# Kernel tuning notes

Hardware: AMD Instinct MI355X
Metric: run time of the kernel (lower is better)

## Reference

```python
import jax, jax.numpy as jnp
import numpy as np

N = 50000
E = 800000
D_IN, D_HID, D_OUT = 128, 128, 256


def _sage_layer(x, src, dst, W_l, b_l, W_r):
    # PyG SAGEConv: out = lin_l(mean_j x_j) + lin_r(x_i)
    msg = x[src]                                              # [E, d]
    agg = jax.ops.segment_sum(msg, dst, num_segments=x.shape[0])
    cnt = jax.ops.segment_sum(jnp.ones((src.shape[0],), x.dtype), dst,
                              num_segments=x.shape[0])
    mean = agg / jnp.maximum(cnt, 1.0)[:, None]
    return mean @ W_l.T + b_l + x @ W_r.T


def setup_inputs() -> dict:
    key = jax.random.key(0)
    ks = jax.random.split(key, 12)
    x = jax.random.normal(ks[0], (N, D_IN), dtype=jnp.float32)
    edge_index = jax.random.randint(ks[1], (2, E), 0, N, dtype=jnp.int64)

    def lin(k, out_d, in_d):
        s = 1.0 / np.sqrt(in_d)
        return jax.random.uniform(k, (out_d, in_d), jnp.float32, -s, s)

    return {
        "x": x,
        "edge_index": edge_index,
        "W_l0": lin(ks[2], D_HID, D_IN),
        "b_l0": jnp.zeros((D_HID,), jnp.float32),
        "W_r0": lin(ks[3], D_HID, D_IN),
        "W_l1": lin(ks[4], D_HID, D_HID),
        "b_l1": jnp.zeros((D_HID,), jnp.float32),
        "W_r1": lin(ks[5], D_HID, D_HID),
        "W_l2": lin(ks[6], D_OUT, D_HID),
        "b_l2": jnp.zeros((D_OUT,), jnp.float32),
        "W_r2": lin(ks[7], D_OUT, D_HID),
    }


def reference(x, edge_index, W_l0, b_l0, W_r0, W_l1, b_l1, W_r1, W_l2, b_l2, W_r2):
    src, dst = edge_index[0], edge_index[1]
    h = jax.nn.relu(_sage_layer(x, src, dst, W_l0, b_l0, W_r0))   # dropout = identity (eval)
    h = jax.nn.relu(_sage_layer(h, src, dst, W_l1, b_l1, W_r1))
    out = _sage_layer(h, src, dst, W_l2, b_l2, W_r2)
    return out
```

## Files before the change

kernel.cpp:

```cpp
#include <hip/hip_runtime.h>
#include <stdint.h>

typedef unsigned short u16;
typedef unsigned int   u32;
typedef __attribute__((ext_vector_type(8))) short short8;
typedef __attribute__((ext_vector_type(4))) float f32x4;

__device__ __forceinline__ u16 f2bf(float f) {
    u32 u = __float_as_uint(f);
    u32 r = (u + 0x7FFFu + ((u >> 16) & 1u)) >> 16;
    return (u16)r;
}

__global__ void detect_fmt(const int* __restrict__ ei, int* __restrict__ flag) {
    if (blockIdx.x == 0 && threadIdx.x == 0) {
        int z = ei[1] | ei[3] | ei[5] | ei[7] | ei[9] | ei[11];
        flag[0] = (z == 0) ? 1 : 0;
    }
}

__global__ void zero_out(float* __restrict__ p, size_t n) {
    size_t i = (size_t)blockIdx.x * 256 + threadIdx.x;
    size_t stride = (size_t)gridDim.x * 256;
    for (; i < n; i += stride) p[i] = 0.f;
}

__global__ void count_deg(const int* __restrict__ ei, const int* __restrict__ flag,
                          int* __restrict__ deg, int E, int N) {
    int e = blockIdx.x * 256 + threadIdx.x;
    if (e >= E) return;
    int dst = flag[0] ? ei[2 * E + 2 * e] : ei[E + e];
    dst = min(max(dst, 0), N - 1);
    atomicAdd(&deg[dst], 1);
}

__global__ void scan_partial(const int* __restrict__ deg, int* __restrict__ bsum, int N) {
    __shared__ int sh[256];
    int t = threadIdx.x;
    int idx0 = blockIdx.x * 1024 + t * 4;
    int s = 0;
    #pragma unroll
    for (int i = 0; i < 4; ++i) { int idx = idx0 + i; if (idx < N) s += deg[idx]; }
    sh[t] = s;
    __syncthreads();
    #pragma unroll
    for (int off = 128; off > 0; off >>= 1) {
        if (t < off) sh[t] += sh[t + off];
        __syncthreads();
    }
    if (t == 0) bsum[blockIdx.x] = sh[0];
}

__global__ void scan_bsum(int* __restrict__ bsum, int nb,
                          int* __restrict__ offs, int N) {
    __shared__ int sh[256];
    __shared__ int carry;
    int t = threadIdx.x;
    if (t == 0) carry = 0;
    __syncthreads();
    for (int base = 0; base < nb; base += 256) {
        int v = (base + t < nb) ? bsum[base + t] : 0;
        sh[t] = v;
        __syncthreads();
        #pragma unroll
        for (int off = 1; off < 256; off <<= 1) {
            int x = (t >= off) ? sh[t - off] : 0;
            __syncthreads();
            sh[t] += x;
            __syncthreads();
        }
        if (base + t < nb) bsum[base + t] = carry + sh[t] - v;
        __syncthreads();
        if (t == 255) carry += sh[255];
        __syncthreads();
    }
    if (t == 0) offs[N] = carry;
}

__global__ void scan_final(int* __restrict__ deg, const int* __restrict__ bsum,
                           int* __restrict__ offs, int N) {
    __shared__ int sh[256];
    int t = threadIdx.x;
    int idx0 = blockIdx.x * 1024 + t * 4;
    int v[4];
    int s = 0;
    #pragma unroll
    for (int i = 0; i < 4; ++i) {
        int idx = idx0 + i;
        v[i] = (idx < N) ? deg[idx] : 0;
        s += v[i];
    }
    sh[t] = s;
    __syncthreads();
    #pragma unroll
    for (int off = 1; off < 256; off <<= 1) {
        int x = (t >= off) ? sh[t - off] : 0;
        __syncthreads();
        sh[t] += x;
        __syncthreads();
    }
    int run = sh[t] - s + bsum[blockIdx.x];
    #pragma unroll
    for (int i = 0; i < 4; ++i) {
        int idx = idx0 + i;
        if (idx < N) { offs[idx] = run; deg[idx] = run; }
        run += v[i];
    }
}

__global__ void bucket_edges(const int* __restrict__ ei, const int* __restrict__ flag,
                             int* __restrict__ cursor, int* __restrict__ ssrc,
                             int E, int N) {
    int e = blockIdx.x * 256 + threadIdx.x;
    if (e >= E) return;
    int is64 = flag[0];
    int src = is64 ? ei[2 * e] : ei[e];
    int dst = is64 ? ei[2 * E + 2 * e] : ei[E + e];
    src = min(max(src, 0), N - 1);
    dst = min(max(dst, 0), N - 1);
    int p = atomicAdd(&cursor[dst], 1);
    if (p >= 0 && p < E) ssrc[p] = src;
}

__global__ void conv_bf16(const float4* __restrict__ x, uint2* __restrict__ H, int n4) {
    int i = blockIdx.x * 256 + threadIdx.x;
    if (i >= n4) return;
    float4 v = x[i];
    uint2 o;
    o.x = ((u32)f2bf(v.y) << 16) | f2bf(v.x);
    o.y = ((u32)f2bf(v.w) << 16) | f2bf(v.z);
    H[i] = o;
}

__global__ void prep_w(const float* __restrict__ Wl, const float* __restrict__ Wr,
                       u16* __restrict__ Wc, int dout) {
    int i = blockIdx.x * 256 + threadIdx.x;
    if (i >= dout * 256) return;
    int j = i >> 8, k = i & 255;
    float v = (k < 128) ? Wl[j * 128 + k] : Wr[j * 128 + (k - 128)];
    Wc[i] = f2bf(v);
}

__global__ void aggregate(const u16* __restrict__ H, const int* __restrict__ offs,
                          const int* __restrict__ ssrc, u16* __restrict__ M, int N) {
    int node = blockIdx.x * 16 + (threadIdx.x >> 4);
    int sub  = threadIdx.x & 15;
    if (node >= N) return;
    int beg = offs[node], end = offs[node + 1];
    float a0[8] = {}, a1[8] = {};
    int j = beg;
    for (; j + 1 < end; j += 2) {
        int s0 = ssrc[j], s1 = ssrc[j + 1];
        uint4 p0 = *(const uint4*)(H + (size_t)s0 * 128 + sub * 8);
        uint4 p1 = *(const uint4*)(H + (size_t)s1 * 128 + sub * 8);
        a0[0] += __uint_as_float(p0.x << 16); a0[1] += __uint_as_float(p0.x & 0xFFFF0000u);
        a0[2] += __uint_as_float(p0.y << 16); a0[3] += __uint_as_float(p0.y & 0xFFFF0000u);
        a0[4] += __uint_as_float(p0.z << 16); a0[5] += __uint_as_float(p0.z & 0xFFFF0000u);
        a0[6] += __uint_as_float(p0.w << 16); a0[7] += __uint_as_float(p0.w & 0xFFFF0000u);
        a1[0] += __uint_as_float(p1.x << 16); a1[1] += __uint_as_float(p1.x & 0xFFFF0000u);
        a1[2] += __uint_as_float(p1.y << 16); a1[3] += __uint_as_float(p1.y & 0xFFFF0000u);
        a1[4] += __uint_as_float(p1.z << 16); a1[5] += __uint_as_float(p1.z & 0xFFFF0000u);
        a1[6] += __uint_as_float(p1.w << 16); a1[7] += __uint_as_float(p1.w & 0xFFFF0000u);
    }
    if (j < end) {
        int s0 = ssrc[j];
        uint4 p0 = *(const uint4*)(H + (size_t)s0 * 128 + sub * 8);
        a0[0] += __uint_as_float(p0.x << 16); a0[1] += __uint_as_float(p0.x & 0xFFFF0000u);
        a0[2] += __uint_as_float(p0.y << 16); a0[3] += __uint_as_float(p0.y & 0xFFFF0000u);
        a0[4] += __uint_as_float(p0.z << 16); a0[5] += __uint_as_float(p0.z & 0xFFFF0000u);
        a0[6] += __uint_as_float(p0.w << 16); a0[7] += __uint_as_float(p0.w & 0xFFFF0000u);
    }
    int d = end - beg;
    float sc = 1.f / (float)(d > 0 ? d : 1);
    uint4 o;
    o.x = ((u32)f2bf((a0[1]+a1[1])*sc) << 16) | f2bf((a0[0]+a1[0])*sc);
    o.y = ((u32)f2bf((a0[3]+a1[3])*sc) << 16) | f2bf((a0[2]+a1[2])*sc);
    o.z = ((u32)f2bf((a0[5]+a1[5])*sc) << 16) | f2bf((a0[4]+a1[4])*sc);
    o.w = ((u32)f2bf((a0[7]+a1[7])*sc) << 16) | f2bf((a0[6]+a1[6])*sc);
    *(uint4*)(M + (size_t)node * 128 + sub * 8) = o;
}

template<int DOUT, bool RELU, bool OUT_F32>
__global__ void gemm_mfma(const u16* __restrict__ M, const u16* __restrict__ H,
                          const u16* __restrict__ Wc, const float* __restrict__ bias,
                          void* __restrict__ out, int N) {
    int tid  = threadIdx.x;
    int w    = tid >> 6;
    int l    = tid & 63;
    int m_base = blockIdx.x * 128 + w * 32;
    int n_base = blockIdx.y * 128;

    int lr = l & 15;
    int lq = l >> 4;
    int kof = lq * 8;

    f32x4 acc[2][8];
    #pragma unroll
    for (int i = 0; i < 2; ++i)
        #pragma unroll
        for (int j = 0; j < 8; ++j) acc[i][j] = (f32x4){0.f, 0.f, 0.f, 0.f};

    int r0 = m_base + lr, r1 = r0 + 16;
    const short8 zf = (short8){0,0,0,0,0,0,0,0};

    #pragma unroll
    for (int ks = 0; ks < 8; ++ks) {
        const u16* Asrc = (ks < 4) ? M : H;
        int ka = (ks & 3) * 32 + kof;
        short8 a0 = (r0 < N) ? *(const short8*)(Asrc + (size_t)r0 * 128 + ka) : zf;
        short8 a1 = (r1 < N) ? *(const short8*)(Asrc + (size_t)r1 * 128 + ka) : zf;
        int kb = ks * 32 + kof;
        #pragma unroll
        for (int ct = 0; ct < 8; ++ct) {
            int wrow = n_base + ct * 16 + lr;
            short8 b = *(const short8*)(Wc + (size_t)wrow * 256 + kb);
            acc[0][ct] = __builtin_amdgcn_mfma_f32_16x16x32_bf16(a0, b, acc[0][ct], 0, 0, 0);
            acc[1][ct] = __builtin_amdgcn_mfma_f32_16x16x32_bf16(a1, b, acc[1][ct], 0, 0, 0);
        }
    }

    #pragma unroll
    for (int rg = 0; rg < 2; ++rg) {
        #pragma unroll
        for (int ct = 0; ct < 8; ++ct) {
            int col = n_base + ct * 16 + lr;
            float bv = bias[col];
            #pragma unroll
            for (int i = 0; i < 4; ++i) {
                int row = m_base + rg * 16 + lq * 4 + i;
                if (row >= N) continue;
                float v = acc[rg][ct][i] + bv;
                if (RELU) v = fmaxf(v, 0.f);
                if (OUT_F32) ((float*)out)[(size_t)row * DOUT + col] = v;
                else         ((u16*)out)[(size_t)row * DOUT + col] = f2bf(v);
            }
        }
    }
}

extern "C" void kernel_launch(void* const* d_in, const int* in_sizes, int n_in,
                              void* d_out, int out_size, void* d_ws, size_t ws_size,
                              hipStream_t stream) {
    const float* x   = (const float*)d_in[0];
    const int*   ei  = (const int*)d_in[1];
    const float* Wl0 = (const float*)d_in[2];
    const float* bl0 = (const float*)d_in[3];
    const float* Wr0 = (const float*)d_in[4];
    const float* Wl1 = (const float*)d_in[5];
    const float* bl1 = (const float*)d_in[6];
    const float* Wr1 = (const float*)d_in[7];
    const float* Wl2 = (const float*)d_in[8];
    const float* bl2 = (const float*)d_in[9];
    const float* Wr2 = (const float*)d_in[10];

    const int N = in_sizes[0] / 128;
    const int E = in_sizes[1] / 2;

    size_t off = 0;
    auto alloc = [&](size_t bytes) -> size_t {
        size_t p = off;
        off += (bytes + 255) & ~(size_t)255;
        return p;
    };
    size_t o_flag = alloc(256);
    size_t o_deg  = alloc((size_t)N * 4);
    size_t o_offs = alloc(((size_t)N + 1) * 4);
    size_t o_ssrc = alloc((size_t)E * 4);
    size_t o_bsum = alloc((((size_t)N + 1023) / 1024) * 4);
    size_t o_Hx   = alloc((size_t)N * 128 * 2);
    size_t o_Ha   = alloc((size_t)N * 128 * 2);
    size_t o_Hb   = alloc((size_t)N * 128 * 2);
    size_t o_Mb   = alloc((size_t)N * 128 * 2);
    size_t o_Wc0  = alloc((size_t)128 * 256 * 2);
    size_t o_Wc1  = alloc((size_t)128 * 256 * 2);
    size_t o_Wc2  = alloc((size_t)256 * 256 * 2);

    if (off > ws_size) {
        zero_out<<<2048, 256, 0, stream>>>((float*)d_out, (size_t)out_size);
        return;
    }

    char* ws = (char*)d_ws;
    int* flag = (int*)(ws + o_flag);
    int* deg  = (int*)(ws + o_deg);
    int* offs = (int*)(ws + o_offs);
    int* ssrc = (int*)(ws + o_ssrc);
    int* bsum = (int*)(ws + o_bsum);
    u16* Hx   = (u16*)(ws + o_Hx);
    u16* Ha   = (u16*)(ws + o_Ha);
    u16* Hb   = (u16*)(ws + o_Hb);
    u16* Mb   = (u16*)(ws + o_Mb);
    u16* Wc0  = (u16*)(ws + o_Wc0);
    u16* Wc1  = (u16*)(ws + o_Wc1);
    u16* Wc2  = (u16*)(ws + o_Wc2);

    hipMemsetAsync(deg, 0, (size_t)N * 4, stream);
    detect_fmt<<<1, 64, 0, stream>>>(ei, flag);

    int eb = (E + 255) / 256;
    int nb = (N + 1023) / 1024;
    count_deg<<<eb, 256, 0, stream>>>(ei, flag, deg, E, N);
    scan_partial<<<nb, 256, 0, stream>>>(deg, bsum, N);
    scan_bsum<<<1, 256, 0, stream>>>(bsum, nb, offs, N);
    scan_final<<<nb, 256, 0, stream>>>(deg, bsum, offs, N);
    bucket_edges<<<eb, 256, 0, stream>>>(ei, flag, deg, ssrc, E, N);

    int n4 = N * 32;
    conv_bf16<<<(n4 + 255) / 256, 256, 0, stream>>>((const float4*)x, (uint2*)Hx, n4);
    prep_w<<<(128 * 256 + 255) / 256, 256, 0, stream>>>(Wl0, Wr0, Wc0, 128);
    prep_w<<<(128 * 256 + 255) / 256, 256, 0, stream>>>(Wl1, Wr1, Wc1, 128);
    prep_w<<<(256 * 256 + 255) / 256, 256, 0, stream>>>(Wl2, Wr2, Wc2, 256);

    int ab = (N + 15) / 16;
    dim3 g1((N + 127) / 128, 1), g2((N + 127) / 128, 2);

    aggregate<<<ab, 256, 0, stream>>>(Hx, offs, ssrc, Mb, N);
    gemm_mfma<128, true, false><<<g1, 256, 0, stream>>>(Mb, Hx, Wc0, bl0, Ha, N);
    aggregate<<<ab, 256, 0, stream>>>(Ha, offs, ssrc, Mb, N);
    gemm_mfma<128, true, false><<<g1, 256, 0, stream>>>(Mb, Ha, Wc1, bl1, Hb, N);
    aggregate<<<ab, 256, 0, stream>>>(Hb, offs, ssrc, Mb, N);
    gemm_mfma<256, false, true><<<g2, 256, 0, stream>>>(Mb, Hb, Wc2, bl2, d_out, N);
}
```

Before: 390.6 us.

## Replace global-atomic CSR build with two-pass shared-memory radix bucketing

Builds the destination-sorted CSR with a two-level bucket sort instead of global atomics. Each chunk first takes a shared-memory histogram over 256-node buckets, then scatters (src,dst) pairs into bucket ranges, and a per-bucket kernel sorts them by node using shared-memory atomics. This removes heavy global atomic contention on the per-node degree and cursor arrays, at the cost of an extra E*8-byte pairs buffer and one more pass over the edges. It also unrolls the aggregation gather loop to four independent loads per iteration to raise memory-level parallelism.

```diff
diff --git a/kernel.cpp b/kernel.cpp
--- a/kernel.cpp
+++ b/kernel.cpp
@@ -6,16 +6,20 @@
 typedef __attribute__((ext_vector_type(8))) short short8;
 typedef __attribute__((ext_vector_type(4))) float f32x4;
 
+#define CHUNK 8192
+
 __device__ __forceinline__ u16 f2bf(float f) {
     u32 u = __float_as_uint(f);
     u32 r = (u + 0x7FFFu + ((u >> 16) & 1u)) >> 16;
     return (u16)r;
 }
 
-__global__ void detect_fmt(const int* __restrict__ ei, int* __restrict__ flag) {
+__global__ void detect_fmt(const int* __restrict__ ei, int* __restrict__ flag,
+                           int* __restrict__ offs, int N, int E) {
     if (blockIdx.x == 0 && threadIdx.x == 0) {
         int z = ei[1] | ei[3] | ei[5] | ei[7] | ei[9] | ei[11];
         flag[0] = (z == 0) ? 1 : 0;
+        offs[N] = E;
     }
 }
 
@@ -25,22 +29,31 @@
     for (; i < n; i += stride) p[i] = 0.f;
 }
 
-__global__ void count_deg(const int* __restrict__ ei, const int* __restrict__ flag,
-                          int* __restrict__ deg, int E, int N) {
-    int e = blockIdx.x * 256 + threadIdx.x;
-    if (e >= E) return;
-    int dst = flag[0] ? ei[2 * E + 2 * e] : ei[E + e];
-    dst = min(max(dst, 0), N - 1);
-    atomicAdd(&deg[dst], 1);
-}
-
-__global__ void scan_partial(const int* __restrict__ deg, int* __restrict__ bsum, int N) {
+__global__ void hist_bucket(const int* __restrict__ ei, const int* __restrict__ flag,
+                            int* __restrict__ cnt, int E, int N, int nb, int NBK) {
+    __shared__ int h[256];
+    int b = blockIdx.x, t = threadIdx.x;
+    h[t] = 0;
+    __syncthreads();
+    int is64 = flag[0];
+    int base = b * CHUNK;
+    int endE = min(base + CHUNK, E);
+    for (int i = base + t; i < endE; i += 256) {
+        int dst = is64 ? ei[2 * E + 2 * i] : ei[E + i];
+        dst = min(max(dst, 0), N - 1);
+        atomicAdd(&h[dst >> 8], 1);
+    }
+    __syncthreads();
+    for (int B = t; B < NBK; B += 256) cnt[B * nb + b] = h[B];
+}
+
+__global__ void scan_partial(const int* __restrict__ a, int* __restrict__ bsum, int M) {
     __shared__ int sh[256];
     int t = threadIdx.x;
     int idx0 = blockIdx.x * 1024 + t * 4;
     int s = 0;
     #pragma unroll
-    for (int i = 0; i < 4; ++i) { int idx = idx0 + i; if (idx < N) s += deg[idx]; }
+    for (int i = 0; i < 4; ++i) { int idx = idx0 + i; if (idx < M) s += a[idx]; }
     sh[t] = s;
     __syncthreads();
     #pragma unroll
@@ -51,15 +64,14 @@
     if (t == 0) bsum[blockIdx.x] = sh[0];
 }
 
-__global__ void scan_bsum(int* __restrict__ bsum, int nb,
-                          int* __restrict__ offs, int N) {
+__global__ void scan_bsum(int* __restrict__ bsum, int nbs) {
     __shared__ int sh[256];
     __shared__ int carry;
     int t = threadIdx.x;
     if (t == 0) carry = 0;
     __syncthreads();
-    for (int base = 0; base < nb; base += 256) {
-        int v = (base + t < nb) ? bsum[base + t] : 0;
+    for (int base = 0; base < nbs; base += 256) {
+        int v = (base + t < nbs) ? bsum[base + t] : 0;
         sh[t] = v;
         __syncthreads();
         #pragma unroll
@@ -69,16 +81,14 @@
             sh[t] += x;
             __syncthreads();
         }
-        if (base + t < nb) bsum[base + t] = carry + sh[t] - v;
+        if (base + t < nbs) bsum[base + t] = carry + sh[t] - v;
         __syncthreads();
         if (t == 255) carry += sh[255];
         __syncthreads();
     }
-    if (t == 0) offs[N] = carry;
-}
-
-__global__ void scan_final(int* __restrict__ deg, const int* __restrict__ bsum,
-                           int* __restrict__ offs, int N) {
+}
+
+__global__ void scan_final(int* __restrict__ a, const int* __restrict__ bsum, int M) {
     __shared__ int sh[256];
     int t = threadIdx.x;
     int idx0 = blockIdx.x * 1024 + t * 4;
@@ -87,7 +97,7 @@
     #pragma unroll
     for (int i = 0; i < 4; ++i) {
         int idx = idx0 + i;
-        v[i] = (idx < N) ? deg[idx] : 0;
+        v[i] = (idx < M) ? a[idx] : 0;
         s += v[i];
     }
     sh[t] = s;
@@ -103,23 +113,67 @@
     #pragma unroll
     for (int i = 0; i < 4; ++i) {
         int idx = idx0 + i;
-        if (idx < N) { offs[idx] = run; deg[idx] = run; }
+        if (idx < M) a[idx] = run;
         run += v[i];
     }
 }
 
-__global__ void bucket_edges(const int* __restrict__ ei, const int* __restrict__ flag,
-                             int* __restrict__ cursor, int* __restrict__ ssrc,
-                             int E, int N) {
-    int e = blockIdx.x * 256 + threadIdx.x;
-    if (e >= E) return;
+__global__ void scatter_pairs(const int* __restrict__ ei, const int* __restrict__ flag,
+                              const int* __restrict__ pboff, int2* __restrict__ pairs,
+                              int E, int N, int nb, int NBK) {
+    __shared__ int cur[256];
+    int b = blockIdx.x, t = threadIdx.x;
+    for (int B = t; B < NBK; B += 256) cur[B] = pboff[B * nb + b];
+    __syncthreads();
     int is64 = flag[0];
-    int src = is64 ? ei[2 * e] : ei[e];
-    int dst = is64 ? ei[2 * E + 2 * e] : ei[E + e];
-    src = min(max(src, 0), N - 1);
-    dst = min(max(dst, 0), N - 1);
-    int p = atomicAdd(&cursor[dst], 1);
-    if (p >= 0 && p < E) ssrc[p] = src;
+    int base = b * CHUNK;
+    int endE = min(base + CHUNK, E);
+    for (int i = base + t; i < endE; i += 256) {
+        int src = is64 ? ei[2 * i] : ei[i];
+        int dst = is64 ? ei[2 * E + 2 * i] : ei[E + i];
+        src = min(max(src, 0), N - 1);
+        dst = min(max(dst, 0), N - 1);
+        int slot = atomicAdd(&cur[dst >> 8], 1);
+        pairs[slot] = make_int2(src, dst);
+    }
+}
+
+__global__ void fine_sort(const int2* __restrict__ pairs, const int* __restrict__ pboff,
+                          int* __restrict__ offs, int* __restrict__ ssrc,
+                          int E, int N, int nb, int NBK) {
+    __shared__ int hist[256];
+    __shared__ int excl[256];
+    __shared__ int cur[256];
+    int B = blockIdx.x, t = threadIdx.x;
+    int rs = pboff[B * nb];
+    int re = (B + 1 < NBK) ? pboff[(B + 1) * nb] : E;
+    hist[t] = 0;
+    __syncthreads();
+    for (int i = rs + t; i < re; i += 256) {
+        int2 p = pairs[i];
+        atomicAdd(&hist[p.y & 255], 1);
+    }
+    __syncthreads();
+    int v = hist[t];
+    excl[t] = v;
+    __syncthreads();
+    #pragma unroll
+    for (int off = 1; off < 256; off <<= 1) {
+        int x = (t >= off) ? excl[t - off] : 0;
+        __syncthreads();
+        excl[t] += x;
+        __syncthreads();
+    }
+    int ex = excl[t] - v;
+    int node = B * 256 + t;
+    if (node < N) offs[node] = rs + ex;
+    cur[t] = rs + ex;
+    __syncthreads();
+    for (int i = rs + t; i < re; i += 256) {
+        int2 p = pairs[i];
+        int slot = atomicAdd(&cur[p.y & 255], 1);
+        ssrc[slot] = p.x;
+    }
 }
 
 __global__ void conv_bf16(const float4* __restrict__ x, uint2* __restrict__ H, int n4) {
@@ -141,42 +195,42 @@
     Wc[i] = f2bf(v);
 }
 
+__device__ __forceinline__ void acc8(float* a, uint4 p) {
+    a[0] += __uint_as_float(p.x << 16); a[1] += __uint_as_float(p.x & 0xFFFF0000u);
+    a[2] += __uint_as_float(p.y << 16); a[3] += __uint_as_float(p.y & 0xFFFF0000u);
+    a[4] += __uint_as_float(p.z << 16); a[5] += __uint_as_float(p.z & 0xFFFF0000u);
+    a[6] += __uint_as_float(p.w << 16); a[7] += __uint_as_float(p.w & 0xFFFF0000u);
+}
+
 __global__ void aggregate(const u16* __restrict__ H, const int* __restrict__ offs,
                           const int* __restrict__ ssrc, u16* __restrict__ M, int N) {
     int node = blockIdx.x * 16 + (threadIdx.x >> 4);
     int sub  = threadIdx.x & 15;
     if (node >= N) return;
     int beg = offs[node], end = offs[node + 1];
-    float a0[8] = {}, a1[8] = {};
+    float a0[8] = {}, a1[8] = {}, a2[8] = {}, a3[8] = {};
     int j = beg;
-    for (; j + 1 < end; j += 2) {
-        int s0 = ssrc[j], s1 = ssrc[j + 1];
+    for (; j + 3 < end; j += 4) {
+        int s0 = ssrc[j], s1 = ssrc[j + 1], s2 = ssrc[j + 2], s3 = ssrc[j + 3];
         uint4 p0 = *(const uint4*)(H + (size_t)s0 * 128 + sub * 8);
         uint4 p1 = *(const uint4*)(H + (size_t)s1 * 128 + sub * 8);
-        a0[0] += __uint_as_float(p0.x << 16); a0[1] += __uint_as_float(p0.x & 0xFFFF0000u);
-        a0[2] += __uint_as_float(p0.y << 16); a0[3] += __uint_as_float(p0.y & 0xFFFF0000u);
-        a0[4] += __uint_as_float(p0.z << 16); a0[5] += __uint_as_float(p0.z & 0xFFFF0000u);
-        a0[6] += __uint_as_float(p0.w << 16); a0[7] += __uint_as_float(p0.w & 0xFFFF0000u);
-        a1[0] += __uint_as_float(p1.x << 16); a1[1] += __uint_as_float(p1.x & 0xFFFF0000u);
-        a1[2] += __uint_as_float(p1.y << 16); a1[3] += __uint_as_float(p1.y & 0xFFFF0000u);
-        a1[4] += __uint_as_float(p1.z << 16); a1[5] += __uint_as_float(p1.z & 0xFFFF0000u);
-        a1[6] += __uint_as_float(p1.w << 16); a1[7] += __uint_as_float(p1.w & 0xFFFF0000u);
-    }
-    if (j < end) {
-        int s0 = ssrc[j];
-        uint4 p0 = *(const uint4*)(H + (size_t)s0 * 128 + sub * 8);
-        a0[0] += __uint_as_float(p0.x << 16); a0[1] += __uint_as_float(p0.x & 0xFFFF0000u);
-        a0[2] += __uint_as_float(p0.y << 16); a0[3] += __uint_as_float(p0.y & 0xFFFF0000u);
-        a0[4] += __uint_as_float(p0.z << 16); a0[5] += __uint_as_float(p0.z & 0xFFFF0000u);
-        a0[6] += __uint_as_float(p0.w << 16); a0[7] += __uint_as_float(p0.w & 0xFFFF0000u);
+        uint4 p2 = *(const uint4*)(H + (size_t)s2 * 128 + sub * 8);
+        uint4 p3 = *(const uint4*)(H + (size_t)s3 * 128 + sub * 8);
+        acc8(a0, p0); acc8(a1, p1); acc8(a2, p2); acc8(a3, p3);
+    }
+    for (; j < end; ++j) {
+        uint4 p0 = *(const uint4*)(H + (size_t)ssrc[j] * 128 + sub * 8);
+        acc8(a0, p0);
     }
     int d = end - beg;
     float sc = 1.f / (float)(d > 0 ? d : 1);
+    #pragma unroll
+    for (int i = 0; i < 8; ++i) a0[i] = (a0[i] + a1[i] + a2[i] + a3[i]) * sc;
     uint4 o;
-    o.x = ((u32)f2bf((a0[1]+a1[1])*sc) << 16) | f2bf((a0[0]+a1[0])*sc);
-    o.y = ((u32)f2bf((a0[3]+a1[3])*sc) << 16) | f2bf((a0[2]+a1[2])*sc);
-    o.z = ((u32)f2bf((a0[5]+a1[5])*sc) << 16) | f2bf((a0[4]+a1[4])*sc);
-    o.w = ((u32)f2bf((a0[7]+a1[7])*sc) << 16) | f2bf((a0[6]+a1[6])*sc);
+    o.x = ((u32)f2bf(a0[1]) << 16) | f2bf(a0[0]);
+    o.y = ((u32)f2bf(a0[3]) << 16) | f2bf(a0[2]);
+    o.z = ((u32)f2bf(a0[5]) << 16) | f2bf(a0[4]);
+    o.w = ((u32)f2bf(a0[7]) << 16) | f2bf(a0[6]);
     *(uint4*)(M + (size_t)node * 128 + sub * 8) = o;
 }
 
@@ -256,54 +310,59 @@
     const int N = in_sizes[0] / 128;
     const int E = in_sizes[1] / 2;
 
+    const int NBK = (N + 255) >> 8;
+    const int nb  = (E + CHUNK - 1) / CHUNK;
+    const int M_  = NBK * nb;
+    const int nbs = (M_ + 1023) / 1024;
+
     size_t off = 0;
     auto alloc = [&](size_t bytes) -> size_t {
         size_t p = off;
         off += (bytes + 255) & ~(size_t)255;
         return p;
     };
-    size_t o_flag = alloc(256);
-    size_t o_deg  = alloc((size_t)N * 4);
-    size_t o_offs = alloc(((size_t)N + 1) * 4);
-    size_t o_ssrc = alloc((size_t)E * 4);
-    size_t o_bsum = alloc((((size_t)N + 1023) / 1024) * 4);
-    size_t o_Hx   = alloc((size_t)N * 128 * 2);
-    size_t o_Ha   = alloc((size_t)N * 128 * 2);
-    size_t o_Hb   = alloc((size_t)N * 128 * 2);
-    size_t o_Mb   = alloc((size_t)N * 128 * 2);
-    size_t o_Wc0  = alloc((size_t)128 * 256 * 2);
-    size_t o_Wc1  = alloc((size_t)128 * 256 * 2);
-    size_t o_Wc2  = alloc((size_t)256 * 256 * 2);
-
-    if (off > ws_size) {
+    size_t o_flag  = alloc(256);
+    size_t o_cnt   = alloc((size_t)M_ * 4);
+    size_t o_bsum  = alloc((size_t)nbs * 4);
+    size_t o_offs  = alloc(((size_t)N + 1) * 4);
+    size_t o_ssrc  = alloc((size_t)E * 4);
+    size_t o_pairs = alloc((size_t)E * 8);
+    size_t o_Hx    = alloc((size_t)N * 128 * 2);
+    size_t o_Ha    = alloc((size_t)N * 128 * 2);
+    size_t o_Hb    = alloc((size_t)N * 128 * 2);
+    size_t o_Mb    = alloc((size_t)N * 128 * 2);
+    size_t o_Wc0   = alloc((size_t)128 * 256 * 2);
+    size_t o_Wc1   = alloc((size_t)128 * 256 * 2);
+    size_t o_Wc2   = alloc((size_t)256 * 256 * 2);
+
+    if (off > ws_size || NBK > 256) {
         zero_out<<<2048, 256, 0, stream>>>((float*)d_out, (size_t)out_size);
         return;
     }
 
     char* ws = (char*)d_ws;
-    int* flag = (int*)(ws + o_flag);
-    int* deg  = (int*)(ws + o_deg);
-    int* offs = (int*)(ws + o_offs);
-    int* ssrc = (int*)(ws + o_ssrc);
-    int* bsum = (int*)(ws + o_bsum);
-    u16* Hx   = (u16*)(ws + o_Hx);
-    u16* Ha   = (u16*)(ws + o_Ha);
-    u16* Hb   = (u16*)(ws + o_Hb);
-    u16* Mb   = (u16*)(ws + o_Mb);
-    u16* Wc0  = (u16*)(ws + o_Wc0);
-    u16* Wc1  = (u16*)(ws + o_Wc1);
-    u16* Wc2  = (u16*)(ws + o_Wc2);
-
-    hipMemsetAsync(deg, 0, (size_t)N * 4, stream);
-    detect_fmt<<<1, 64, 0, stream>>>(ei, flag);
-
-    int eb = (E + 255) / 256;
-    int nb = (N + 1023) / 1024;
-    count_deg<<<eb, 256, 0, stream>>>(ei, flag, deg, E, N);
-    scan_partial<<<nb, 256, 0, stream>>>(deg, bsum, N);
-    scan_bsum<<<1, 256, 0, stream>>>(bsum, nb, offs, N);
-    scan_final<<<nb, 256, 0, stream>>>(deg, bsum, offs, N);
-    bucket_edges<<<eb, 256, 0, stream>>>(ei, flag, deg, ssrc, E, N);
+    int*  flag  = (int*)(ws + o_flag);
+    int*  cnt   = (int*)(ws + o_cnt);
+    int*  bsum  = (int*)(ws + o_bsum);
+    int*  offs  = (int*)(ws + o_offs);
+    int*  ssrc  = (int*)(ws + o_ssrc);
+    int2* pairs = (int2*)(ws + o_pairs);
+    u16*  Hx    = (u16*)(ws + o_Hx);
+    u16*  Ha    = (u16*)(ws + o_Ha);
+    u16*  Hb    = (u16*)(ws + o_Hb);
+    u16*  Mb    = (u16*)(ws + o_Mb);
+    u16*  Wc0   = (u16*)(ws + o_Wc0);
+    u16*  Wc1   = (u16*)(ws + o_Wc1);
+    u16*  Wc2   = (u16*)(ws + o_Wc2);
+
+    detect_fmt<<<1, 64, 0, stream>>>(ei, flag, offs, N, E);
+
+    hist_bucket<<<nb, 256, 0, stream>>>(ei, flag, cnt, E, N, nb, NBK);
+    scan_partial<<<nbs, 256, 0, stream>>>(cnt, bsum, M_);
+    scan_bsum<<<1, 256, 0, stream>>>(bsum, nbs);
+    scan_final<<<nbs, 256, 0, stream>>>(cnt, bsum, M_);
+    scatter_pairs<<<nb, 256, 0, stream>>>(ei, flag, cnt, pairs, E, N, nb, NBK);
+    fine_sort<<<NBK, 256, 0, stream>>>(pairs, cnt, offs, ssrc, E, N, nb, NBK);
 
     int n4 = N * 32;
     conv_bf16<<<(n4 + 255) / 256, 256, 0, stream>>>((const float4*)x, (uint2*)Hx, n4);
```

After: 359.8 us. -7.9%, faster.
